# Performance work log

Hardware: AMD Instinct MI355X
Metric: run time of the kernel (lower is better)

The kernel has to match this reference:

```python
import jax, jax.numpy as jnp
import numpy as np

PROCESSING_SPEED = 8.0  # init kwarg: softmax temperature
EPS = 1e-8              # torch F.cosine_similarity eps
BATCH, SIZE, DIM = 1024, 65536, 512


def setup_inputs() -> dict:
    key = jax.random.key(0)
    k1, k2 = jax.random.split(key)
    x = jax.random.normal(k1, (BATCH, DIM), dtype=jnp.float32)
    memory_bank = jax.random.normal(k2, (SIZE, DIM), dtype=jnp.float32)
    return {"x": x, "memory_bank": memory_bank}


def reference(x, memory_bank):
    # Cosine similarity between every query and every memory row, computed as
    # normalized dot products (math-equivalent to F.cosine_similarity with
    # denominator clamp max(||a||*||b||, eps), avoiding the (B,S,D) broadcast).
    x_norm = jnp.linalg.norm(x, axis=1, keepdims=True)            # (B, 1)
    m_norm = jnp.linalg.norm(memory_bank, axis=1, keepdims=True)  # (S, 1)
    dots = jnp.einsum('bd,sd->bs', x, memory_bank)                # (B, S)
    sims = dots / jnp.maximum(x_norm * m_norm.T, EPS)             # (B, S)
    attention = jax.nn.softmax(sims * PROCESSING_SPEED, axis=1)   # (B, S)
    return attention @ memory_bank                                # (B, D)
```

## Files before the change

kernel.cpp:

```cpp
#include <hip/hip_runtime.h>
#include <hip/hip_bf16.h>
#include <stdint.h>

#define B_N 1024
#define S_N 65536
#define D_N 512
#define NS 32
#define SC (S_N / NS)
#define SB 128
#define NSUB (SC / SB)

typedef __attribute__((ext_vector_type(8))) short bf16x8;
typedef __attribute__((ext_vector_type(4))) float f32x4;

#define OFF_MBF   ((size_t)0)
#define OFF_MT    (OFF_MBF + (size_t)S_N * D_N * 2)
#define OFF_XBF   (OFF_MT  + (size_t)D_N * S_N * 2)
#define OFF_RX    (OFF_XBF + (size_t)B_N * D_N * 2)
#define OFF_RM    (OFF_RX  + (size_t)B_N * 4)
#define OFF_LSUM  (OFF_RM  + (size_t)S_N * 4)
#define OFF_OPART (OFF_LSUM + (size_t)B_N * 4)

__device__ __forceinline__ unsigned short f2bf(float f) {
  unsigned u = __builtin_bit_cast(unsigned, f);
  u += 0x7fffu + ((u >> 16) & 1u);
  return (unsigned short)(u >> 16);
}

__device__ __forceinline__ void stage16(const unsigned short* g, unsigned short* l) {
  __builtin_amdgcn_global_load_lds(
      (const __attribute__((address_space(1))) void*)g,
      (__attribute__((address_space(3))) void*)l, 16, 0, 0);
}

__global__ void k_prep_x(const float* __restrict__ X, unsigned short* __restrict__ Xbf,
                         float* __restrict__ rx) {
  const int row = blockIdx.x;
  const int t = threadIdx.x;
  float4 v = ((const float4*)(X + (size_t)row * D_N))[t];
  float ss = v.x*v.x + v.y*v.y + v.z*v.z + v.w*v.w;
  ushort4 o; o.x = f2bf(v.x); o.y = f2bf(v.y); o.z = f2bf(v.z); o.w = f2bf(v.w);
  ((ushort4*)(Xbf + (size_t)row * D_N))[t] = o;
  #pragma unroll
  for (int m = 1; m < 64; m <<= 1) ss += __shfl_xor(ss, m);
  __shared__ float partial[2];
  if ((t & 63) == 0) partial[t >> 6] = ss;
  __syncthreads();
  if (t == 0) rx[row] = 11.541560327111707f * rsqrtf(fmaxf(partial[0] + partial[1], 1e-24f));
}

__global__ void k_prep_m(const float* __restrict__ M, unsigned short* __restrict__ Mbf,
                         unsigned short* __restrict__ Mt, float* __restrict__ rm) {
  __shared__ float ts[64 * 65];
  const int t = threadIdx.x;
  const int s0 = blockIdx.x * 64;
  const int r = t >> 2, cq = t & 3;
  const int c = t >> 2, sq = t & 3;
  float ss = 0.f;
  for (int ct = 0; ct < 8; ++ct) {
    float f[16];
    const float4* src = (const float4*)(M + (size_t)(s0 + r) * D_N + ct * 64 + cq * 16);
    #pragma unroll
    for (int k = 0; k < 4; ++k) {
      float4 v = src[k];
      f[4*k+0] = v.x; f[4*k+1] = v.y; f[4*k+2] = v.z; f[4*k+3] = v.w;
    }
    union { unsigned short u[16]; uint4 v4[2]; } pk;
    #pragma unroll
    for (int j = 0; j < 16; ++j) {
      ss += f[j] * f[j];
      pk.u[j] = f2bf(f[j]);
      ts[r * 65 + cq * 16 + j] = f[j];
    }
    uint4* dst = (uint4*)(Mbf + (size_t)(s0 + r) * D_N + ct * 64 + cq * 16);
    dst[0] = pk.v4[0]; dst[1] = pk.v4[1];
    __syncthreads();
    union { unsigned short u[16]; uint4 v4[2]; } pt;
    #pragma unroll
    for (int j = 0; j < 16; ++j) pt.u[j] = f2bf(ts[(sq * 16 + j) * 65 + c]);
    uint4* dt = (uint4*)(Mt + (size_t)(ct * 64 + c) * S_N + s0 + sq * 16);
    dt[0] = pt.v4[0]; dt[1] = pt.v4[1];
    __syncthreads();
  }
  ss += __shfl_xor(ss, 1);
  ss += __shfl_xor(ss, 2);
  if (cq == 0) rm[s0 + r] = rsqrtf(fmaxf(ss, 1e-24f));
}

__global__ __launch_bounds__(512, 2) void k_fused(
    const unsigned short* __restrict__ Xbf, const unsigned short* __restrict__ Mbf,
    const unsigned short* __restrict__ Mt, const float* __restrict__ rx,
    const float* __restrict__ rminv, float* __restrict__ lsum,
    float* __restrict__ Opart) {
  __shared__ unsigned short smem[16384];
  __shared__ unsigned short Ps[16384];

  const int t = threadIdx.x;
  const int w = t >> 6, lane = t & 63, quad = lane >> 4, l15 = lane & 15;
  const int qr = w >> 1, qc = w & 1;
  const int x7 = l15 & 7;

  const int bid = blockIdx.x;
  const int xcd = bid & 7, slot = bid >> 3;
  const int bblk = slot & 7;
  const int chunk = xcd * 4 + (slot >> 3);
  const int b0 = bblk * 128;
  const int s0 = chunk * SC;

  unsigned short* As = smem;
  unsigned short* Bs = smem + 8192;

  f32x4 accO[4][2][4];
  #pragma unroll
  for (int dc = 0; dc < 4; ++dc)
    #pragma unroll
    for (int i = 0; i < 2; ++i)
      #pragma unroll
      for (int j = 0; j < 4; ++j) accO[dc][i][j] = (f32x4){0.f, 0.f, 0.f, 0.f};

  float ls[4] = {0.f, 0.f, 0.f, 0.f};
  float rxj[4];
  #pragma unroll
  for (int j = 0; j < 4; ++j) rxj[j] = rx[b0 + qc * 64 + j * 16 + l15];

  const int srow8 = t >> 3;
  const int sch8  = ((t & 7) ^ (srow8 & 7)) * 8;
  const unsigned short* gX = Xbf + (size_t)(b0 + srow8) * D_N + sch8;
  const int mrow = t >> 4;
  const int mch  = ((t & 15) ^ (mrow & 7)) * 8;

  for (int sub = 0; sub < NSUB; ++sub) {
    const int sS = s0 + sub * SB;

    f32x4 accP[2][4];
    #pragma unroll
    for (int i = 0; i < 2; ++i)
      #pragma unroll
      for (int j = 0; j < 4; ++j) accP[i][j] = (f32x4){0.f, 0.f, 0.f, 0.f};

    const unsigned short* gM = Mbf + (size_t)(sS + srow8) * D_N + sch8;
    for (int k0 = 0; k0 < D_N; k0 += 64) {
      stage16(gM + k0,                      As + w * 512);
      stage16(gM + (size_t)64 * D_N + k0,   As + 4096 + w * 512);
      stage16(gX + k0,                      Bs + w * 512);
      stage16(gX + (size_t)64 * D_N + k0,   Bs + 4096 + w * 512);
      __syncthreads();
      #pragma unroll
      for (int kk = 0; kk < 64; kk += 32) {
        const int cq = (kk >> 3) + quad;
        bf16x8 a[2], b[4];
        #pragma unroll
        for (int i = 0; i < 2; ++i)
          a[i] = *(const bf16x8*)&As[(qr * 32 + i * 16 + l15) * 64 + ((cq ^ x7) << 3)];
        #pragma unroll
        for (int j = 0; j < 4; ++j)
          b[j] = *(const bf16x8*)&Bs[(qc * 64 + j * 16 + l15) * 64 + ((cq ^ x7) << 3)];
        #pragma unroll
        for (int i = 0; i < 2; ++i)
          #pragma unroll
          for (int j = 0; j < 4; ++j)
            accP[i][j] = __builtin_amdgcn_mfma_f32_16x16x32_bf16(a[i], b[j], accP[i][j], 0, 0, 0);
      }
      __syncthreads();
    }

    const float4 rm0 = *(const float4*)&rminv[sS + qr * 32 + quad * 4];
    const float4 rm1 = *(const float4*)&rminv[sS + qr * 32 + 16 + quad * 4];
    #pragma unroll
    for (int i = 0; i < 2; ++i) {
      const float4 rm = i ? rm1 : rm0;
      const int sl  = qr * 32 + i * 16 + quad * 4;
      const int c16 = sl >> 3;
      const int o8  = (sl >> 2) & 1;
      #pragma unroll
      for (int j = 0; j < 4; ++j) {
        const float p0 = exp2f(accP[i][j][0] * rxj[j] * rm.x);
        const float p1 = exp2f(accP[i][j][1] * rxj[j] * rm.y);
        const float p2 = exp2f(accP[i][j][2] * rxj[j] * rm.z);
        const float p3 = exp2f(accP[i][j][3] * rxj[j] * rm.w);
        ls[j] += (p0 + p1) + (p2 + p3);
        const int brow = qc * 64 + j * 16 + l15;
        uint2 pk;
        pk.x = (unsigned)f2bf(p0) | ((unsigned)f2bf(p1) << 16);
        pk.y = (unsigned)f2bf(p2) | ((unsigned)f2bf(p3) << 16);
        *(uint2*)&Ps[brow * 128 + (((c16 ^ (brow & 7)) << 3) | (o8 << 2))] = pk;
      }
    }
    __syncthreads();

    #pragma unroll
    for (int dc = 0; dc < 4; ++dc) {
      const unsigned short* gT = Mt + (size_t)(dc * 128 + mrow) * S_N + sS + mch;
      stage16(gT,                      smem + w * 512);
      stage16(gT + (size_t)32 * S_N,   smem + 4096 + w * 512);
      stage16(gT + (size_t)64 * S_N,   smem + 8192 + w * 512);
      stage16(gT + (size_t)96 * S_N,   smem + 12288 + w * 512);
      __syncthreads();
      #pragma unroll
      for (int kk = 0; kk < 128; kk += 32) {
        const int cq = (kk >> 3) + quad;
        bf16x8 pa[2], mb[4];
        #pragma unroll
        for (int i = 0; i < 2; ++i)
          pa[i] = *(const bf16x8*)&Ps[(qr * 32 + i * 16 + l15) * 128 + ((cq ^ x7) << 3)];
        #pragma unroll
        for (int j = 0; j < 4; ++j)
          mb[j] = *(const bf16x8*)&smem[(qc * 64 + j * 16 + l15) * 128 + ((cq ^ x7) << 3)];
        #pragma unroll
        for (int i = 0; i < 2; ++i)
          #pragma unroll
          for (int j = 0; j < 4; ++j)
            accO[dc][i][j] = __builtin_amdgcn_mfma_f32_16x16x32_bf16(pa[i], mb[j], accO[dc][i][j], 0, 0, 0);
      }
      __syncthreads();
    }
  }

  float* Od = Opart + (size_t)chunk * ((size_t)B_N * D_N);
  #pragma unroll
  for (int dc = 0; dc < 4; ++dc)
    #pragma unroll
    for (int i = 0; i < 2; ++i)
      #pragma unroll
      for (int r = 0; r < 4; ++r) {
        const int bb = b0 + qr * 32 + i * 16 + quad * 4 + r;
        #pragma unroll
        for (int j = 0; j < 4; ++j) {
          const int d = dc * 128 + qc * 64 + j * 16 + l15;
          Od[(size_t)bb * D_N + d] = accO[dc][i][j][r];
        }
      }

  __syncthreads();
  float* red = (float*)smem;
  #pragma unroll
  for (int j = 0; j < 4; ++j) {
    float v = ls[j];
    v += __shfl_xor(v, 16);
    v += __shfl_xor(v, 32);
    if (lane < 16) red[w * 64 + j * 16 + lane] = v;
  }
  __syncthreads();
  if (t < 128) {
    const int qc2 = t >> 6, idx = t & 63;
    float s = red[(0 + qc2) * 64 + idx] + red[(2 + qc2) * 64 + idx] +
              red[(4 + qc2) * 64 + idx] + red[(6 + qc2) * 64 + idx];
    unsafeAtomicAdd(&lsum[b0 + t], s);
  }
}

__global__ void k_combine(const float* __restrict__ Opart, const float* __restrict__ lsum,
                          float* __restrict__ out) {
  const int idx = blockIdx.x * 256 + threadIdx.x;
  const int b = idx >> 7;
  float4 s = {0.f, 0.f, 0.f, 0.f};
  #pragma unroll
  for (int ks = 0; ks < NS; ++ks) {
    float4 v = ((const float4*)Opart)[(size_t)ks * (B_N * D_N / 4) + idx];
    s.x += v.x; s.y += v.y; s.z += v.z; s.w += v.w;
  }
  const float inv = 1.0f / lsum[b];
  s.x *= inv; s.y *= inv; s.z *= inv; s.w *= inv;
  ((float4*)out)[idx] = s;
}

extern "C" void kernel_launch(void* const* d_in, const int* in_sizes, int n_in,
                              void* d_out, int out_size, void* d_ws, size_t ws_size,
                              hipStream_t stream) {
  const float* X = (const float*)d_in[0];
  const float* M = (const float*)d_in[1];
  char* ws = (char*)d_ws;
  unsigned short* Mbf = (unsigned short*)(ws + OFF_MBF);
  unsigned short* Mt  = (unsigned short*)(ws + OFF_MT);
  unsigned short* Xbf = (unsigned short*)(ws + OFF_XBF);
  float* rxv  = (float*)(ws + OFF_RX);
  float* rmv  = (float*)(ws + OFF_RM);
  float* lsum = (float*)(ws + OFF_LSUM);
  float* Opart = (float*)(ws + OFF_OPART);

  hipMemsetAsync(lsum, 0, B_N * sizeof(float), stream);
  k_prep_x<<<dim3(B_N), 128, 0, stream>>>(X, Xbf, rxv);
  k_prep_m<<<dim3(S_N / 64), 256, 0, stream>>>(M, Mbf, Mt, rmv);
  k_fused<<<dim3(8 * NS), 512, 0, stream>>>(Xbf, Mbf, Mt, rxv, rmv, lsum, Opart);
  k_combine<<<dim3(B_N * D_N / 4 / 256), 256, 0, stream>>>(Opart, lsum, (float*)d_out);
}
```

Baseline: 468.8 us.

## Double-buffer LDS staging and prefetch across the QK and PV stages

Doubles the shared staging buffer so the next tile's global-to-LDS copy is issued before the current tile's MFMA work. The prefetch chain crosses stage boundaries: the last QK step prefetches the first PV tile, and the last PV step prefetches the next sub-block's first QK tile. Full __syncthreads are replaced by partial vmcnt waits plus raw s_barrier, and s_setprio is raised around the MFMA loops. The goal is to hide global load latency behind matrix math. The cost is more LDS per block, which can lower occupancy, and a fragile reliance on exact outstanding-load counts.

Result: faster. 429.6 us (-8.4%).

```diff
diff --git a/kernel.cpp b/kernel.cpp
--- a/kernel.cpp
+++ b/kernel.cpp
@@ -92,7 +92,7 @@
     const unsigned short* __restrict__ Mt, const float* __restrict__ rx,
     const float* __restrict__ rminv, float* __restrict__ lsum,
     float* __restrict__ Opart) {
-  __shared__ unsigned short smem[16384];
+  __shared__ unsigned short sbuf[2][16384];
   __shared__ unsigned short Ps[16384];
 
   const int t = threadIdx.x;
@@ -107,9 +107,6 @@
   const int b0 = bblk * 128;
   const int s0 = chunk * SC;
 
-  unsigned short* As = smem;
-  unsigned short* Bs = smem + 8192;
-
   f32x4 accO[4][2][4];
   #pragma unroll
   for (int dc = 0; dc < 4; ++dc)
@@ -125,9 +122,33 @@
 
   const int srow8 = t >> 3;
   const int sch8  = ((t & 7) ^ (srow8 & 7)) * 8;
-  const unsigned short* gX = Xbf + (size_t)(b0 + srow8) * D_N + sch8;
+  const unsigned short* gX0 = Xbf + (size_t)(b0 + srow8) * D_N + sch8;
+  const unsigned short* gM0 = Mbf + (size_t)srow8 * D_N + sch8;
   const int mrow = t >> 4;
   const int mch  = ((t & 15) ^ (mrow & 7)) * 8;
+  const unsigned short* gT0 = Mt + (size_t)mrow * S_N + mch;
+
+  #define ISSUE_QK(sS_, k0_, bi_) do {                                       \
+    unsigned short* bA_ = &sbuf[(bi_)][0];                                   \
+    unsigned short* bB_ = &sbuf[(bi_)][8192];                                \
+    const unsigned short* gM_ = gM0 + (size_t)(sS_) * D_N + (k0_);           \
+    stage16(gM_,                   bA_ + w * 512);                           \
+    stage16(gM_ + (size_t)64*D_N,  bA_ + 4096 + w * 512);                    \
+    const unsigned short* gX_ = gX0 + (k0_);                                 \
+    stage16(gX_,                   bB_ + w * 512);                           \
+    stage16(gX_ + (size_t)64*D_N,  bB_ + 4096 + w * 512);                    \
+  } while (0)
+
+  #define ISSUE_PV(sS_, dc_, bi_) do {                                       \
+    unsigned short* bT_ = &sbuf[(bi_)][0];                                   \
+    const unsigned short* gT_ = gT0 + (size_t)((dc_) * 128) * S_N + (sS_);   \
+    stage16(gT_,                   bT_ + w * 512);                           \
+    stage16(gT_ + (size_t)32*S_N,  bT_ + 4096 + w * 512);                    \
+    stage16(gT_ + (size_t)64*S_N,  bT_ + 8192 + w * 512);                    \
+    stage16(gT_ + (size_t)96*S_N,  bT_ + 12288 + w * 512);                   \
+  } while (0)
+
+  ISSUE_QK(s0, 0, 0);
 
   for (int sub = 0; sub < NSUB; ++sub) {
     const int sS = s0 + sub * SB;
@@ -138,13 +159,16 @@
       #pragma unroll
       for (int j = 0; j < 4; ++j) accP[i][j] = (f32x4){0.f, 0.f, 0.f, 0.f};
 
-    const unsigned short* gM = Mbf + (size_t)(sS + srow8) * D_N + sch8;
-    for (int k0 = 0; k0 < D_N; k0 += 64) {
-      stage16(gM + k0,                      As + w * 512);
-      stage16(gM + (size_t)64 * D_N + k0,   As + 4096 + w * 512);
-      stage16(gX + k0,                      Bs + w * 512);
-      stage16(gX + (size_t)64 * D_N + k0,   Bs + 4096 + w * 512);
-      __syncthreads();
+    #pragma unroll
+    for (int st = 0; st < 8; ++st) {
+      const int bi = st & 1;
+      if (st < 7) { ISSUE_QK(sS, (st + 1) * 64, bi ^ 1); }
+      else        { ISSUE_PV(sS, 0, bi ^ 1); }
+      asm volatile("s_waitcnt vmcnt(4)" ::: "memory");
+      __builtin_amdgcn_s_barrier();
+      const unsigned short* As = &sbuf[bi][0];
+      const unsigned short* Bs = &sbuf[bi][8192];
+      __builtin_amdgcn_s_setprio(1);
       #pragma unroll
       for (int kk = 0; kk < 64; kk += 32) {
         const int cq = (kk >> 3) + quad;
@@ -161,41 +185,46 @@
           for (int j = 0; j < 4; ++j)
             accP[i][j] = __builtin_amdgcn_mfma_f32_16x16x32_bf16(a[i], b[j], accP[i][j], 0, 0, 0);
       }
-      __syncthreads();
-    }
-
-    const float4 rm0 = *(const float4*)&rminv[sS + qr * 32 + quad * 4];
-    const float4 rm1 = *(const float4*)&rminv[sS + qr * 32 + 16 + quad * 4];
-    #pragma unroll
-    for (int i = 0; i < 2; ++i) {
-      const float4 rm = i ? rm1 : rm0;
-      const int sl  = qr * 32 + i * 16 + quad * 4;
-      const int c16 = sl >> 3;
-      const int o8  = (sl >> 2) & 1;
-      #pragma unroll
-      for (int j = 0; j < 4; ++j) {
-        const float p0 = exp2f(accP[i][j][0] * rxj[j] * rm.x);
-        const float p1 = exp2f(accP[i][j][1] * rxj[j] * rm.y);
-        const float p2 = exp2f(accP[i][j][2] * rxj[j] * rm.z);
-        const float p3 = exp2f(accP[i][j][3] * rxj[j] * rm.w);
-        ls[j] += (p0 + p1) + (p2 + p3);
-        const int brow = qc * 64 + j * 16 + l15;
-        uint2 pk;
-        pk.x = (unsigned)f2bf(p0) | ((unsigned)f2bf(p1) << 16);
-        pk.y = (unsigned)f2bf(p2) | ((unsigned)f2bf(p3) << 16);
-        *(uint2*)&Ps[brow * 128 + (((c16 ^ (brow & 7)) << 3) | (o8 << 2))] = pk;
+      __builtin_amdgcn_s_setprio(0);
+      __builtin_amdgcn_s_barrier();
+    }
+
+    {
+      const float4 rm0 = *(const float4*)&rminv[sS + qr * 32 + quad * 4];
+      const float4 rm1 = *(const float4*)&rminv[sS + qr * 32 + 16 + quad * 4];
+      #pragma unroll
+      for (int i = 0; i < 2; ++i) {
+        const float4 rm = i ? rm1 : rm0;
+        const int sl  = qr * 32 + i * 16 + quad * 4;
+        const int c16 = sl >> 3;
+        const int o8  = (sl >> 2) & 1;
+        #pragma unroll
+        for (int j = 0; j < 4; ++j) {
+          const float p0 = exp2f(accP[i][j][0] * rxj[j] * rm.x);
+          const float p1 = exp2f(accP[i][j][1] * rxj[j] * rm.y);
+          const float p2 = exp2f(accP[i][j][2] * rxj[j] * rm.z);
+          const float p3 = exp2f(accP[i][j][3] * rxj[j] * rm.w);
+          ls[j] += (p0 + p1) + (p2 + p3);
+          const int brow = qc * 64 + j * 16 + l15;
+          uint2 pk;
+          pk.x = (unsigned)f2bf(p0) | ((unsigned)f2bf(p1) << 16);
+          pk.y = (unsigned)f2bf(p2) | ((unsigned)f2bf(p3) << 16);
+          *(uint2*)&Ps[brow * 128 + (((c16 ^ (brow & 7)) << 3) | (o8 << 2))] = pk;
+        }
       }
-    }
-    __syncthreads();
+      asm volatile("s_waitcnt lgkmcnt(0)" ::: "memory");
+    }
 
     #pragma unroll
     for (int dc = 0; dc < 4; ++dc) {
-      const unsigned short* gT = Mt + (size_t)(dc * 128 + mrow) * S_N + sS + mch;
-      stage16(gT,                      smem + w * 512);
-      stage16(gT + (size_t)32 * S_N,   smem + 4096 + w * 512);
-      stage16(gT + (size_t)64 * S_N,   smem + 8192 + w * 512);
-      stage16(gT + (size_t)96 * S_N,   smem + 12288 + w * 512);
-      __syncthreads();
+      const int bi = dc & 1;
+      if (dc < 3)                  { ISSUE_PV(sS, dc + 1, bi ^ 1); }
+      else if (sub < NSUB - 1)     { ISSUE_QK(sS + SB, 0, bi ^ 1); }
+      if (dc == 3 && sub == NSUB - 1) asm volatile("s_waitcnt vmcnt(0)" ::: "memory");
+      else                            asm volatile("s_waitcnt vmcnt(4)" ::: "memory");
+      __builtin_amdgcn_s_barrier();
+      const unsigned short* Tsb = &sbuf[bi][0];
+      __builtin_amdgcn_s_setprio(1);
       #pragma unroll
       for (int kk = 0; kk < 128; kk += 32) {
         const int cq = (kk >> 3) + quad;
@@ -205,14 +234,15 @@
           pa[i] = *(const bf16x8*)&Ps[(qr * 32 + i * 16 + l15) * 128 + ((cq ^ x7) << 3)];
         #pragma unroll
         for (int j = 0; j < 4; ++j)
-          mb[j] = *(const bf16x8*)&smem[(qc * 64 + j * 16 + l15) * 128 + ((cq ^ x7) << 3)];
+          mb[j] = *(const bf16x8*)&Tsb[(qc * 64 + j * 16 + l15) * 128 + ((cq ^ x7) << 3)];
         #pragma unroll
         for (int i = 0; i < 2; ++i)
           #pragma unroll
           for (int j = 0; j < 4; ++j)
             accO[dc][i][j] = __builtin_amdgcn_mfma_f32_16x16x32_bf16(pa[i], mb[j], accO[dc][i][j], 0, 0, 0);
       }
-      __syncthreads();
+      __builtin_amdgcn_s_setprio(0);
+      __builtin_amdgcn_s_barrier();
     }
   }
 
@@ -232,7 +262,7 @@
       }
 
   __syncthreads();
-  float* red = (float*)smem;
+  float* red = (float*)&sbuf[0][0];
   #pragma unroll
   for (int j = 0; j < 4; ++j) {
     float v = ls[j];
@@ -247,6 +277,8 @@
               red[(4 + qc2) * 64 + idx] + red[(6 + qc2) * 64 + idx];
     unsafeAtomicAdd(&lsum[b0 + t], s);
   }
+  #undef ISSUE_QK
+  #undef ISSUE_PV
 }
 
 __global__ void k_combine(const float* __restrict__ Opart, const float* __restrict__ lsum,
```

## Double-buffer global-to-LDS loads and enlarge the S sub-tile to 256 rows

Applied to the files above, without the earlier changes.

Doubles the per-iteration S sub-tile to 256 and reorganises both GEMM phases into 8-step loops with double-buffered LDS staging. The next tile's M, X or Mt loads are issued before computing on the current one, with explicit vmcnt waits and raw barriers replacing syncthreads, plus setprio around the MFMA bursts. Warp tiles grow to 64x64 so each fragment load feeds more MFMAs. The costs are doubled LDS usage (64KB for Mb, 64KB for Ps), more accumulator registers, and tricky hand-counted vmcnt values that could race if the issue order is wrong.

Result: slower. 543.2 us (+15.9%).

```diff
diff --git a/kernel.cpp b/kernel.cpp
--- a/kernel.cpp
+++ b/kernel.cpp
@@ -7,7 +7,7 @@
 #define D_N 512
 #define NS 32
 #define SC (S_N / NS)
-#define SB 128
+#define SB 256
 #define NSUB (SC / SB)
 
 typedef __attribute__((ext_vector_type(8))) short bf16x8;
@@ -92,12 +92,13 @@
     const unsigned short* __restrict__ Mt, const float* __restrict__ rx,
     const float* __restrict__ rminv, float* __restrict__ lsum,
     float* __restrict__ Opart) {
-  __shared__ unsigned short smem[16384];
-  __shared__ unsigned short Ps[16384];
+  __shared__ unsigned short Mb[2][16384];
+  __shared__ unsigned short Ps[32768];
 
   const int t = threadIdx.x;
   const int w = t >> 6, lane = t & 63, quad = lane >> 4, l15 = lane & 15;
-  const int qr = w >> 1, qc = w & 1;
+  const int qs = w >> 1, qcb = w & 1;
+  const int qb = w >> 2, qd = w & 3;
   const int x7 = l15 & 7;
 
   const int bid = blockIdx.x;
@@ -107,132 +108,163 @@
   const int b0 = bblk * 128;
   const int s0 = chunk * SC;
 
-  unsigned short* As = smem;
-  unsigned short* Bs = smem + 8192;
-
-  f32x4 accO[4][2][4];
-  #pragma unroll
-  for (int dc = 0; dc < 4; ++dc)
-    #pragma unroll
-    for (int i = 0; i < 2; ++i)
-      #pragma unroll
-      for (int j = 0; j < 4; ++j) accO[dc][i][j] = (f32x4){0.f, 0.f, 0.f, 0.f};
+  f32x4 accO[2][4][4];
+  #pragma unroll
+  for (int g = 0; g < 2; ++g)
+    #pragma unroll
+    for (int i = 0; i < 4; ++i)
+      #pragma unroll
+      for (int j = 0; j < 4; ++j) accO[g][i][j] = (f32x4){0.f, 0.f, 0.f, 0.f};
 
   float ls[4] = {0.f, 0.f, 0.f, 0.f};
   float rxj[4];
   #pragma unroll
-  for (int j = 0; j < 4; ++j) rxj[j] = rx[b0 + qc * 64 + j * 16 + l15];
+  for (int j = 0; j < 4; ++j) rxj[j] = rx[b0 + qcb * 64 + j * 16 + l15];
 
   const int srow8 = t >> 3;
   const int sch8  = ((t & 7) ^ (srow8 & 7)) * 8;
   const unsigned short* gX = Xbf + (size_t)(b0 + srow8) * D_N + sch8;
-  const int mrow = t >> 4;
-  const int mch  = ((t & 15) ^ (mrow & 7)) * 8;
+  const unsigned short* gM = Mbf + (size_t)srow8 * D_N + sch8;
+  const unsigned short* gT = Mt  + (size_t)srow8 * S_N + sch8;
+  unsigned short* MbU = &Mb[0][0];
+
+  #define ISS_M(sS_, k0_, bi_) do {                                           \
+    _Pragma("unroll")                                                         \
+    for (int is = 0; is < 4; ++is)                                            \
+      stage16(gM + (size_t)((sS_) + is * 64) * D_N + (k0_),                   \
+              MbU + (bi_) * 16384 + is * 4096 + w * 512);                     \
+  } while (0)
+  #define ISS_X(k0_, bi_) do {                                                \
+    _Pragma("unroll")                                                         \
+    for (int is = 0; is < 2; ++is)                                            \
+      stage16(gX + (size_t)(is * 64) * D_N + (k0_),                           \
+              Ps + (bi_) * 8192 + is * 4096 + w * 512);                       \
+  } while (0)
+  #define ISS_T(sS_, p_, bi_) do {                                            \
+    _Pragma("unroll")                                                         \
+    for (int is = 0; is < 4; ++is)                                            \
+      stage16(gT + (size_t)(((p_) >> 2) * 256 + is * 64) * S_N + (sS_) + (((p_) & 3) * 64), \
+              MbU + (bi_) * 16384 + is * 4096 + w * 512);                     \
+  } while (0)
+
+  ISS_M(s0, 0, 0);
+  ISS_X(0, 0);
 
   for (int sub = 0; sub < NSUB; ++sub) {
     const int sS = s0 + sub * SB;
 
-    f32x4 accP[2][4];
-    #pragma unroll
-    for (int i = 0; i < 2; ++i)
+    f32x4 accP[4][4];
+    #pragma unroll
+    for (int i = 0; i < 4; ++i)
       #pragma unroll
       for (int j = 0; j < 4; ++j) accP[i][j] = (f32x4){0.f, 0.f, 0.f, 0.f};
 
-    const unsigned short* gM = Mbf + (size_t)(sS + srow8) * D_N + sch8;
-    for (int k0 = 0; k0 < D_N; k0 += 64) {
-      stage16(gM + k0,                      As + w * 512);
-      stage16(gM + (size_t)64 * D_N + k0,   As + 4096 + w * 512);
-      stage16(gX + k0,                      Bs + w * 512);
-      stage16(gX + (size_t)64 * D_N + k0,   Bs + 4096 + w * 512);
-      __syncthreads();
+    #pragma unroll
+    for (int p = 0; p < 8; ++p) {
+      const int bi = p & 1;
+      if (p < 7) { ISS_M(sS, (p + 1) * 64, bi ^ 1); ISS_X((p + 1) * 64, bi ^ 1); }
+      else       { ISS_T(sS, 0, 0); }
+      if (p < 7) asm volatile("s_waitcnt vmcnt(6)" ::: "memory");
+      else       asm volatile("s_waitcnt vmcnt(4)" ::: "memory");
+      __builtin_amdgcn_s_barrier();
+      const unsigned short* As = MbU + bi * 16384;
+      const unsigned short* Xs = Ps + bi * 8192;
+      __builtin_amdgcn_s_setprio(1);
       #pragma unroll
       for (int kk = 0; kk < 64; kk += 32) {
-        const int cq = (kk >> 3) + quad;
-        bf16x8 a[2], b[4];
-        #pragma unroll
-        for (int i = 0; i < 2; ++i)
-          a[i] = *(const bf16x8*)&As[(qr * 32 + i * 16 + l15) * 64 + ((cq ^ x7) << 3)];
+        const int c = (kk >> 3) + quad;
+        bf16x8 a[4], b[4];
+        #pragma unroll
+        for (int i = 0; i < 4; ++i)
+          a[i] = *(const bf16x8*)&As[(qs * 64 + i * 16 + l15) * 64 + ((c ^ x7) << 3)];
         #pragma unroll
         for (int j = 0; j < 4; ++j)
-          b[j] = *(const bf16x8*)&Bs[(qc * 64 + j * 16 + l15) * 64 + ((cq ^ x7) << 3)];
-        #pragma unroll
-        for (int i = 0; i < 2; ++i)
+          b[j] = *(const bf16x8*)&Xs[(qcb * 64 + j * 16 + l15) * 64 + ((c ^ x7) << 3)];
+        #pragma unroll
+        for (int i = 0; i < 4; ++i)
           #pragma unroll
           for (int j = 0; j < 4; ++j)
             accP[i][j] = __builtin_amdgcn_mfma_f32_16x16x32_bf16(a[i], b[j], accP[i][j], 0, 0, 0);
       }
-      __syncthreads();
-    }
-
-    const float4 rm0 = *(const float4*)&rminv[sS + qr * 32 + quad * 4];
-    const float4 rm1 = *(const float4*)&rminv[sS + qr * 32 + 16 + quad * 4];
-    #pragma unroll
-    for (int i = 0; i < 2; ++i) {
-      const float4 rm = i ? rm1 : rm0;
-      const int sl  = qr * 32 + i * 16 + quad * 4;
-      const int c16 = sl >> 3;
-      const int o8  = (sl >> 2) & 1;
-      #pragma unroll
-      for (int j = 0; j < 4; ++j) {
-        const float p0 = exp2f(accP[i][j][0] * rxj[j] * rm.x);
-        const float p1 = exp2f(accP[i][j][1] * rxj[j] * rm.y);
-        const float p2 = exp2f(accP[i][j][2] * rxj[j] * rm.z);
-        const float p3 = exp2f(accP[i][j][3] * rxj[j] * rm.w);
-        ls[j] += (p0 + p1) + (p2 + p3);
-        const int brow = qc * 64 + j * 16 + l15;
-        uint2 pk;
-        pk.x = (unsigned)f2bf(p0) | ((unsigned)f2bf(p1) << 16);
-        pk.y = (unsigned)f2bf(p2) | ((unsigned)f2bf(p3) << 16);
-        *(uint2*)&Ps[brow * 128 + (((c16 ^ (brow & 7)) << 3) | (o8 << 2))] = pk;
+      __builtin_amdgcn_s_setprio(0);
+      __builtin_amdgcn_s_barrier();
+    }
+
+    {
+      #pragma unroll
+      for (int i = 0; i < 4; ++i) {
+        const float4 rm = *(const float4*)&rminv[sS + qs * 64 + i * 16 + quad * 4];
+        const int c16 = qs * 8 + i * 2 + (quad >> 1);
+        #pragma unroll
+        for (int j = 0; j < 4; ++j) {
+          const float p0 = exp2f(accP[i][j][0] * rxj[j] * rm.x);
+          const float p1 = exp2f(accP[i][j][1] * rxj[j] * rm.y);
+          const float p2 = exp2f(accP[i][j][2] * rxj[j] * rm.z);
+          const float p3 = exp2f(accP[i][j][3] * rxj[j] * rm.w);
+          ls[j] += (p0 + p1) + (p2 + p3);
+          const int brow = qcb * 64 + j * 16 + l15;
+          uint2 pk;
+          pk.x = (unsigned)f2bf(p0) | ((unsigned)f2bf(p1) << 16);
+          pk.y = (unsigned)f2bf(p2) | ((unsigned)f2bf(p3) << 16);
+          *(uint2*)&Ps[brow * 256 + (((c16 ^ (brow & 7)) << 3) | ((quad & 1) << 2))] = pk;
+        }
       }
-    }
-    __syncthreads();
-
-    #pragma unroll
-    for (int dc = 0; dc < 4; ++dc) {
-      const unsigned short* gT = Mt + (size_t)(dc * 128 + mrow) * S_N + sS + mch;
-      stage16(gT,                      smem + w * 512);
-      stage16(gT + (size_t)32 * S_N,   smem + 4096 + w * 512);
-      stage16(gT + (size_t)64 * S_N,   smem + 8192 + w * 512);
-      stage16(gT + (size_t)96 * S_N,   smem + 12288 + w * 512);
-      __syncthreads();
-      #pragma unroll
-      for (int kk = 0; kk < 128; kk += 32) {
-        const int cq = (kk >> 3) + quad;
-        bf16x8 pa[2], mb[4];
-        #pragma unroll
-        for (int i = 0; i < 2; ++i)
-          pa[i] = *(const bf16x8*)&Ps[(qr * 32 + i * 16 + l15) * 128 + ((cq ^ x7) << 3)];
+      asm volatile("s_waitcnt lgkmcnt(0)" ::: "memory");
+      __builtin_amdgcn_sched_barrier(0);
+    }
+
+    #pragma unroll
+    for (int p = 0; p < 8; ++p) {
+      const int bi = p & 1;
+      if (p < 7)                 { ISS_T(sS, p + 1, bi ^ 1); }
+      else if (sub < NSUB - 1)   { ISS_M(sS + SB, 0, 0); }
+      if (p == 7 && sub == NSUB - 1) asm volatile("s_waitcnt vmcnt(0)" ::: "memory");
+      else                           asm volatile("s_waitcnt vmcnt(4)" ::: "memory");
+      __builtin_amdgcn_s_barrier();
+      const unsigned short* Ts = MbU + bi * 16384;
+      const int dcg = p >> 2;
+      __builtin_amdgcn_s_setprio(1);
+      #pragma unroll
+      for (int kk = 0; kk < 64; kk += 32) {
+        const int cP = (((p & 3) * 64 + kk) >> 3) + quad;
+        const int cT = (kk >> 3) + quad;
+        bf16x8 pa[4], mb[4];
+        #pragma unroll
+        for (int i = 0; i < 4; ++i)
+          pa[i] = *(const bf16x8*)&Ps[(qb * 64 + i * 16 + l15) * 256 + ((cP ^ x7) << 3)];
         #pragma unroll
         for (int j = 0; j < 4; ++j)
-          mb[j] = *(const bf16x8*)&smem[(qc * 64 + j * 16 + l15) * 128 + ((cq ^ x7) << 3)];
-        #pragma unroll
-        for (int i = 0; i < 2; ++i)
+          mb[j] = *(const bf16x8*)&Ts[(qd * 64 + j * 16 + l15) * 64 + ((cT ^ x7) << 3)];
+        #pragma unroll
+        for (int i = 0; i < 4; ++i)
           #pragma unroll
           for (int j = 0; j < 4; ++j)
-            accO[dc][i][j] = __builtin_amdgcn_mfma_f32_16x16x32_bf16(pa[i], mb[j], accO[dc][i][j], 0, 0, 0);
+            accO[dcg][i][j] = __builtin_amdgcn_mfma_f32_16x16x32_bf16(pa[i], mb[j], accO[dcg][i][j], 0, 0, 0);
       }
-      __syncthreads();
-    }
+      __builtin_amdgcn_s_setprio(0);
+      __builtin_amdgcn_s_barrier();
+    }
+
+    if (sub < NSUB - 1) { ISS_X(0, 0); }
   }
 
   float* Od = Opart + (size_t)chunk * ((size_t)B_N * D_N);
   #pragma unroll
-  for (int dc = 0; dc < 4; ++dc)
-    #pragma unroll
-    for (int i = 0; i < 2; ++i)
+  for (int g = 0; g < 2; ++g)
+    #pragma unroll
+    for (int i = 0; i < 4; ++i)
       #pragma unroll
       for (int r = 0; r < 4; ++r) {
-        const int bb = b0 + qr * 32 + i * 16 + quad * 4 + r;
+        const int bb = b0 + qb * 64 + i * 16 + quad * 4 + r;
         #pragma unroll
         for (int j = 0; j < 4; ++j) {
-          const int d = dc * 128 + qc * 64 + j * 16 + l15;
-          Od[(size_t)bb * D_N + d] = accO[dc][i][j][r];
+          const int d = g * 256 + qd * 64 + j * 16 + l15;
+          Od[(size_t)bb * D_N + d] = accO[g][i][j][r];
         }
       }
 
   __syncthreads();
-  float* red = (float*)smem;
+  float* red = (float*)MbU;
   #pragma unroll
   for (int j = 0; j < 4; ++j) {
     float v = ls[j];
@@ -247,6 +279,9 @@
               red[(4 + qc2) * 64 + idx] + red[(6 + qc2) * 64 + idx];
     unsafeAtomicAdd(&lsum[b0 + t], s);
   }
+  #undef ISS_M
+  #undef ISS_X
+  #undef ISS_T
 }
 
 __global__ void k_combine(const float* __restrict__ Opart, const float* __restrict__ lsum,
```

## Restructure fused kernel: resident X tile, direct-to-register M loads, larger warp tiles

Applied to the files above, without the earlier changes.

The fused attention kernel now uses 256 threads per block and loads the whole 128x512 X tile into LDS once. M (for the dot products) and the transposed M (for the output GEMM) are read straight from global memory into registers with double buffering, and no longer staged through LDS. Each wave owns a larger 64x64 similarity tile and a 128x128 output tile, so there are fewer barriers and more MFMAs per fragment load. The cost is much higher register pressure (accO alone is 256 floats per thread), a single wave group per block, and uncoalesced global loads that skip LDS swizzling. That could cause spills or expose memory latency.

Result: slower. 700.0 us (+49.3%).

```diff
diff --git a/kernel.cpp b/kernel.cpp
--- a/kernel.cpp
+++ b/kernel.cpp
@@ -87,17 +87,17 @@
   if (cq == 0) rm[s0 + r] = rsqrtf(fmaxf(ss, 1e-24f));
 }
 
-__global__ __launch_bounds__(512, 2) void k_fused(
+__global__ __launch_bounds__(256, 1) void k_fused(
     const unsigned short* __restrict__ Xbf, const unsigned short* __restrict__ Mbf,
     const unsigned short* __restrict__ Mt, const float* __restrict__ rx,
     const float* __restrict__ rminv, float* __restrict__ lsum,
     float* __restrict__ Opart) {
-  __shared__ unsigned short smem[16384];
-  __shared__ unsigned short Ps[16384];
+  __shared__ unsigned short Xs[128 * 512];
+  __shared__ unsigned short Ps[128 * 128];
 
   const int t = threadIdx.x;
   const int w = t >> 6, lane = t & 63, quad = lane >> 4, l15 = lane & 15;
-  const int qr = w >> 1, qc = w & 1;
+  const int qs2 = w >> 1, qb2 = w & 1;
   const int x7 = l15 & 7;
 
   const int bid = blockIdx.x;
@@ -107,71 +107,71 @@
   const int b0 = bblk * 128;
   const int s0 = chunk * SC;
 
-  unsigned short* As = smem;
-  unsigned short* Bs = smem + 8192;
-
-  f32x4 accO[4][2][4];
-  #pragma unroll
-  for (int dc = 0; dc < 4; ++dc)
-    #pragma unroll
-    for (int i = 0; i < 2; ++i)
-      #pragma unroll
-      for (int j = 0; j < 4; ++j) accO[dc][i][j] = (f32x4){0.f, 0.f, 0.f, 0.f};
+  #pragma unroll
+  for (int i = 0; i < 32; ++i) {
+    const int row = i * 4 + w;
+    stage16(Xbf + (size_t)(b0 + row) * D_N + ((lane ^ (row & 7)) << 3),
+            Xs + i * 2048 + w * 512);
+  }
+  asm volatile("s_waitcnt vmcnt(0)" ::: "memory");
+  __builtin_amdgcn_s_barrier();
+
+  f32x4 accO[8][8];
+  #pragma unroll
+  for (int i = 0; i < 8; ++i)
+    #pragma unroll
+    for (int j = 0; j < 8; ++j) accO[i][j] = (f32x4){0.f, 0.f, 0.f, 0.f};
 
   float ls[4] = {0.f, 0.f, 0.f, 0.f};
   float rxj[4];
   #pragma unroll
-  for (int j = 0; j < 4; ++j) rxj[j] = rx[b0 + qc * 64 + j * 16 + l15];
-
-  const int srow8 = t >> 3;
-  const int sch8  = ((t & 7) ^ (srow8 & 7)) * 8;
-  const unsigned short* gX = Xbf + (size_t)(b0 + srow8) * D_N + sch8;
-  const int mrow = t >> 4;
-  const int mch  = ((t & 15) ^ (mrow & 7)) * 8;
+  for (int j = 0; j < 4; ++j) rxj[j] = rx[b0 + qb2 * 64 + j * 16 + l15];
+
+  const unsigned short* gT0 = Mt + (size_t)(w * 128 + l15) * S_N + (size_t)s0 + quad * 8;
 
   for (int sub = 0; sub < NSUB; ++sub) {
     const int sS = s0 + sub * SB;
 
-    f32x4 accP[2][4];
-    #pragma unroll
-    for (int i = 0; i < 2; ++i)
+    f32x4 accP[4][4];
+    #pragma unroll
+    for (int i = 0; i < 4; ++i)
       #pragma unroll
       for (int j = 0; j < 4; ++j) accP[i][j] = (f32x4){0.f, 0.f, 0.f, 0.f};
 
-    const unsigned short* gM = Mbf + (size_t)(sS + srow8) * D_N + sch8;
-    for (int k0 = 0; k0 < D_N; k0 += 64) {
-      stage16(gM + k0,                      As + w * 512);
-      stage16(gM + (size_t)64 * D_N + k0,   As + 4096 + w * 512);
-      stage16(gX + k0,                      Bs + w * 512);
-      stage16(gX + (size_t)64 * D_N + k0,   Bs + 4096 + w * 512);
-      __syncthreads();
-      #pragma unroll
-      for (int kk = 0; kk < 64; kk += 32) {
-        const int cq = (kk >> 3) + quad;
-        bf16x8 a[2], b[4];
-        #pragma unroll
-        for (int i = 0; i < 2; ++i)
-          a[i] = *(const bf16x8*)&As[(qr * 32 + i * 16 + l15) * 64 + ((cq ^ x7) << 3)];
+    const unsigned short* gM = Mbf + (size_t)(sS + qs2 * 64 + l15) * D_N + quad * 8;
+    const int xrow = qb2 * 64 + l15;
+
+    bf16x8 aB[2][4], xB[2][4];
+    #pragma unroll
+    for (int i = 0; i < 4; ++i)
+      aB[0][i] = *(const bf16x8*)(gM + (size_t)(i * 16) * D_N);
+    #pragma unroll
+    for (int j = 0; j < 4; ++j)
+      xB[0][j] = *(const bf16x8*)&Xs[(xrow + j * 16) * 512 + ((quad ^ x7) << 3)];
+
+    #pragma unroll
+    for (int ks = 0; ks < 16; ++ks) {
+      const int cur = ks & 1, nxt = cur ^ 1;
+      if (ks < 15) {
+        #pragma unroll
+        for (int i = 0; i < 4; ++i)
+          aB[nxt][i] = *(const bf16x8*)(gM + (size_t)(i * 16) * D_N + (ks + 1) * 32);
+        const int c = (ks + 1) * 4 + quad;
         #pragma unroll
         for (int j = 0; j < 4; ++j)
-          b[j] = *(const bf16x8*)&Bs[(qc * 64 + j * 16 + l15) * 64 + ((cq ^ x7) << 3)];
-        #pragma unroll
-        for (int i = 0; i < 2; ++i)
-          #pragma unroll
-          for (int j = 0; j < 4; ++j)
-            accP[i][j] = __builtin_amdgcn_mfma_f32_16x16x32_bf16(a[i], b[j], accP[i][j], 0, 0, 0);
-      }
-      __syncthreads();
-    }
-
-    const float4 rm0 = *(const float4*)&rminv[sS + qr * 32 + quad * 4];
-    const float4 rm1 = *(const float4*)&rminv[sS + qr * 32 + 16 + quad * 4];
-    #pragma unroll
-    for (int i = 0; i < 2; ++i) {
-      const float4 rm = i ? rm1 : rm0;
-      const int sl  = qr * 32 + i * 16 + quad * 4;
-      const int c16 = sl >> 3;
-      const int o8  = (sl >> 2) & 1;
+          xB[nxt][j] = *(const bf16x8*)&Xs[(xrow + j * 16) * 512 + ((c ^ x7) << 3)];
+      }
+      #pragma unroll
+      for (int i = 0; i < 4; ++i)
+        #pragma unroll
+        for (int j = 0; j < 4; ++j)
+          accP[i][j] = __builtin_amdgcn_mfma_f32_16x16x32_bf16(aB[cur][i], xB[cur][j], accP[i][j], 0, 0, 0);
+    }
+
+    #pragma unroll
+    for (int i = 0; i < 4; ++i) {
+      const float4 rm = *(const float4*)&rminv[sS + qs2 * 64 + i * 16 + quad * 4];
+      const int c16 = qs2 * 8 + i * 2 + (quad >> 1);
       #pragma unroll
       for (int j = 0; j < 4; ++j) {
         const float p0 = exp2f(accP[i][j][0] * rxj[j] * rm.x);
@@ -179,60 +179,62 @@
         const float p2 = exp2f(accP[i][j][2] * rxj[j] * rm.z);
         const float p3 = exp2f(accP[i][j][3] * rxj[j] * rm.w);
         ls[j] += (p0 + p1) + (p2 + p3);
-        const int brow = qc * 64 + j * 16 + l15;
+        const int brow = qb2 * 64 + j * 16 + l15;
         uint2 pk;
         pk.x = (unsigned)f2bf(p0) | ((unsigned)f2bf(p1) << 16);
         pk.y = (unsigned)f2bf(p2) | ((unsigned)f2bf(p3) << 16);
-        *(uint2*)&Ps[brow * 128 + (((c16 ^ (brow & 7)) << 3) | (o8 << 2))] = pk;
-      }
-    }
-    __syncthreads();
-
-    #pragma unroll
-    for (int dc = 0; dc < 4; ++dc) {
-      const unsigned short* gT = Mt + (size_t)(dc * 128 + mrow) * S_N + sS + mch;
-      stage16(gT,                      smem + w * 512);
-      stage16(gT + (size_t)32 * S_N,   smem + 4096 + w * 512);
-      stage16(gT + (size_t)64 * S_N,   smem + 8192 + w * 512);
-      stage16(gT + (size_t)96 * S_N,   smem + 12288 + w * 512);
-      __syncthreads();
-      #pragma unroll
-      for (int kk = 0; kk < 128; kk += 32) {
-        const int cq = (kk >> 3) + quad;
-        bf16x8 pa[2], mb[4];
-        #pragma unroll
-        for (int i = 0; i < 2; ++i)
-          pa[i] = *(const bf16x8*)&Ps[(qr * 32 + i * 16 + l15) * 128 + ((cq ^ x7) << 3)];
-        #pragma unroll
-        for (int j = 0; j < 4; ++j)
-          mb[j] = *(const bf16x8*)&smem[(qc * 64 + j * 16 + l15) * 128 + ((cq ^ x7) << 3)];
-        #pragma unroll
-        for (int i = 0; i < 2; ++i)
-          #pragma unroll
-          for (int j = 0; j < 4; ++j)
-            accO[dc][i][j] = __builtin_amdgcn_mfma_f32_16x16x32_bf16(pa[i], mb[j], accO[dc][i][j], 0, 0, 0);
-      }
-      __syncthreads();
-    }
+        *(uint2*)&Ps[brow * 128 + (((c16 ^ x7) << 3) | ((quad & 1) << 2))] = pk;
+      }
+    }
+    asm volatile("s_waitcnt lgkmcnt(0)" ::: "memory");
+    __builtin_amdgcn_s_barrier();
+
+    const unsigned short* gT = gT0 + sub * SB;
+    bf16x8 mB[2][8], pB[2][8];
+    #pragma unroll
+    for (int j = 0; j < 8; ++j)
+      mB[0][j] = *(const bf16x8*)(gT + (size_t)(j * 16) * S_N);
+    #pragma unroll
+    for (int i = 0; i < 8; ++i)
+      pB[0][i] = *(const bf16x8*)&Ps[(i * 16 + l15) * 128 + ((quad ^ x7) << 3)];
+
+    #pragma unroll
+    for (int kk = 0; kk < 4; ++kk) {
+      const int cur = kk & 1, nxt = cur ^ 1;
+      if (kk < 3) {
+        #pragma unroll
+        for (int j = 0; j < 8; ++j)
+          mB[nxt][j] = *(const bf16x8*)(gT + (size_t)(j * 16) * S_N + (kk + 1) * 32);
+        const int c = (kk + 1) * 4 + quad;
+        #pragma unroll
+        for (int i = 0; i < 8; ++i)
+          pB[nxt][i] = *(const bf16x8*)&Ps[(i * 16 + l15) * 128 + ((c ^ x7) << 3)];
+      }
+      #pragma unroll
+      for (int i = 0; i < 8; ++i)
+        #pragma unroll
+        for (int j = 0; j < 8; ++j)
+          accO[i][j] = __builtin_amdgcn_mfma_f32_16x16x32_bf16(pB[cur][i], mB[cur][j], accO[i][j], 0, 0, 0);
+    }
+    asm volatile("s_waitcnt lgkmcnt(0)" ::: "memory");
+    __builtin_amdgcn_s_barrier();
   }
 
   float* Od = Opart + (size_t)chunk * ((size_t)B_N * D_N);
   #pragma unroll
-  for (int dc = 0; dc < 4; ++dc)
-    #pragma unroll
-    for (int i = 0; i < 2; ++i)
-      #pragma unroll
-      for (int r = 0; r < 4; ++r) {
-        const int bb = b0 + qr * 32 + i * 16 + quad * 4 + r;
-        #pragma unroll
-        for (int j = 0; j < 4; ++j) {
-          const int d = dc * 128 + qc * 64 + j * 16 + l15;
-          Od[(size_t)bb * D_N + d] = accO[dc][i][j][r];
-        }
-      }
+  for (int i = 0; i < 8; ++i)
+    #pragma unroll
+    for (int r = 0; r < 4; ++r) {
+      const int bb = b0 + i * 16 + quad * 4 + r;
+      #pragma unroll
+      for (int j = 0; j < 8; ++j) {
+        const int d = w * 128 + j * 16 + l15;
+        Od[(size_t)bb * D_N + d] = accO[i][j][r];
+      }
+    }
 
   __syncthreads();
-  float* red = (float*)smem;
+  float* red = (float*)Ps;
   #pragma unroll
   for (int j = 0; j < 4; ++j) {
     float v = ls[j];
@@ -242,9 +244,7 @@
   }
   __syncthreads();
   if (t < 128) {
-    const int qc2 = t >> 6, idx = t & 63;
-    float s = red[(0 + qc2) * 64 + idx] + red[(2 + qc2) * 64 + idx] +
-              red[(4 + qc2) * 64 + idx] + red[(6 + qc2) * 64 + idx];
+    float s = red[t] + red[t + 128];
     unsafeAtomicAdd(&lsum[b0 + t], s);
   }
 }
@@ -281,6 +281,6 @@
   hipMemsetAsync(lsum, 0, B_N * sizeof(float), stream);
   k_prep_x<<<dim3(B_N), 128, 0, stream>>>(X, Xbf, rxv);
   k_prep_m<<<dim3(S_N / 64), 256, 0, stream>>>(M, Mbf, Mt, rmv);
-  k_fused<<<dim3(8 * NS), 512, 0, stream>>>(Xbf, Mbf, Mt, rxv, rmv, lsum, Opart);
+  k_fused<<<dim3(8 * NS), 256, 0, stream>>>(Xbf, Mbf, Mt, rxv, rmv, lsum, Opart);
   k_combine<<<dim3(B_N * D_N / 4 / 256), 256, 0, stream>>>(Opart, lsum, (float*)d_out);
 }
```
